# Kernel optimization log

Measured on AMD Instinct MI355X. Metric: run time of the kernel, lower is better.

## Reference

```python
import jax, jax.numpy as jnp
import numpy as np

EPS = 1e-12  # torch.nn.functional.normalize default eps


def sage_conv(x, src, dst, W_l, W_r, b, n_nodes):
    # PyG SAGEConv (mean aggr): out = lin_l(mean_{j in N(i)} x_j) + lin_r(x_i)
    # messages flow src -> dst
    agg = jax.ops.segment_sum(x[src], dst, num_segments=n_nodes)           # [N, d_in]
    cnt = jax.ops.segment_sum(jnp.ones_like(dst, dtype=x.dtype), dst,
                              num_segments=n_nodes)                         # [N]
    mean = agg / jnp.maximum(cnt, 1.0)[:, None]
    return mean @ W_l + x @ W_r + b


def l2_normalize(x):
    n = jnp.linalg.norm(x, axis=-1, keepdims=True)
    return x / jnp.maximum(n, EPS)


def setup_inputs() -> dict:
    key = jax.random.key(0)
    ks = jax.random.split(key, 16)
    N, E, G = 50000, 800000, 64
    d_in, d_h, d_out = 128, 128, 128

    x = jax.random.normal(ks[0], (N, d_in), dtype=jnp.float32)
    edge_index = jax.random.randint(ks[1], (2, E), 0, N, dtype=jnp.int32)
    batch = jnp.sort(jax.random.randint(ks[2], (N,), 0, G, dtype=jnp.int32))

    def lin(k, fan_in, fan_out):
        bound = 1.0 / np.sqrt(fan_in)
        return jax.random.uniform(k, (fan_in, fan_out), jnp.float32, -bound, bound)

    params = {
        "W_l1": lin(ks[3], d_in, d_h), "W_r1": lin(ks[4], d_in, d_h),
        "b1": jnp.zeros((d_h,), jnp.float32),
        "W_l2": lin(ks[5], d_h, d_h), "W_r2": lin(ks[6], d_h, d_h),
        "b2": jnp.zeros((d_h,), jnp.float32),
        "W_l3": lin(ks[7], d_h, d_out), "W_r3": lin(ks[8], d_h, d_out),
        "b3": jnp.zeros((d_out,), jnp.float32),
    }
    return {"x": x, "edge_index": edge_index, "batch": batch, **params}


def reference(x, edge_index, batch,
              W_l1, W_r1, b1, W_l2, W_r2, b2, W_l3, W_r3, b3):
    N = x.shape[0]
    G = 64  # number of graphs in the batch
    src, dst = edge_index[0], edge_index[1]

    h = jax.nn.relu(sage_conv(x, src, dst, W_l1, W_r1, b1, N))
    h = l2_normalize(h)
    h = jax.nn.relu(sage_conv(h, src, dst, W_l2, W_r2, b2, N))
    h = l2_normalize(h)
    h = sage_conv(h, src, dst, W_l3, W_r3, b3, N)
    h = l2_normalize(h)

    # global mean pool over graphs
    summed = jax.ops.segment_sum(h, batch, num_segments=G)                 # [G, d_out]
    counts = jax.ops.segment_sum(jnp.ones((N,), h.dtype), batch, num_segments=G)
    return summed / jnp.maximum(counts, 1.0)[:, None]
```

## Files before the change

### kernel.cpp

```cpp
#include <hip/hip_runtime.h>

#define N_NODES 50000
#define N_EDGES 800000
#define DIM 128
#define N_GRAPHS 64
#define NTILES 3125
#define NB 196
#define GPART 256
#define EPB 3125
#define XBF_BLKS 6250

typedef __attribute__((ext_vector_type(8))) short short8;
typedef __attribute__((ext_vector_type(4))) float f32x4;

__device__ __forceinline__ float bf2f(unsigned short h) {
  unsigned int u = ((unsigned int)h) << 16;
  return __builtin_bit_cast(float, u);
}
__device__ __forceinline__ unsigned short f2bf(float f) {
  unsigned int u = __builtin_bit_cast(unsigned int, f);
  u += 0x7FFFu + ((u >> 16) & 1u);
  return (unsigned short)(u >> 16);
}

__global__ __launch_bounds__(256) void k_front(
    const int* __restrict__ ei, int* __restrict__ cnt,
    const float* __restrict__ x, unsigned short* __restrict__ xbf,
    const float* __restrict__ w0, const float* __restrict__ w1,
    const float* __restrict__ w2, const float* __restrict__ w3,
    const float* __restrict__ w4, const float* __restrict__ w5,
    unsigned short* __restrict__ wfrag, float* __restrict__ out,
    const int* __restrict__ batch, float* __restrict__ inv_gcnt) {
  int blk = blockIdx.x, tid = threadIdx.x;
  if (blk < GPART) {
    __shared__ int h[NB];
    if (tid < NB) h[tid] = 0;
    __syncthreads();
    int e0 = blk * EPB;
    for (int i = tid; i < EPB; i += 256) {
      int dst = ei[N_EDGES + e0 + i];
      atomicAdd(&h[dst >> 8], 1);
    }
    __syncthreads();
    if (tid < NB) cnt[blk * NB + tid] = h[tid];
  } else if (blk < GPART + XBF_BLKS) {
    int i = (blk - GPART) * 256 + tid;
    if (i * 4 >= N_NODES * DIM) return;
    float4 v = ((const float4*)x)[i];
    unsigned int lo = (unsigned int)f2bf(v.x) | ((unsigned int)f2bf(v.y) << 16);
    unsigned int hi = (unsigned int)f2bf(v.z) | ((unsigned int)f2bf(v.w) << 16);
    uint2 o; o.x = lo; o.y = hi;
    ((uint2*)xbf)[i] = o;
  } else {
    int b = blk - GPART - XBF_BLKS;
    if (b < 48) {
      int idx = b * 256 + tid;
      int mat = idx >> 11;
      int rem = idx & 2047;
      int lane = rem & 63;
      int kk = (rem >> 6) & 3;
      int t = rem >> 8;
      const float* w = (mat == 0) ? w0 : (mat == 1) ? w1 : (mat == 2) ? w2
                     : (mat == 3) ? w3 : (mat == 4) ? w4 : w5;
      int row = t * 16 + (lane & 15);
      int k0 = kk * 32 + (lane >> 4) * 8;
      unsigned int v[8];
      #pragma unroll
      for (int j = 0; j < 8; ++j) v[j] = f2bf(w[(k0 + j) * DIM + row]);
      uint4 o;
      o.x = v[0] | (v[1] << 16);
      o.y = v[2] | (v[3] << 16);
      o.z = v[4] | (v[5] << 16);
      o.w = v[6] | (v[7] << 16);
      ((uint4*)wfrag)[idx] = o;
    } else if (b < 80) {
      int i = (b - 48) * 256 + tid;
      if (i < N_GRAPHS * DIM) out[i] = 0.f;
    } else {
      int g = tid;
      if (g >= N_GRAPHS) return;
      int lo = 0, hi = N_NODES;
      while (lo < hi) { int m = (lo + hi) >> 1; if (batch[m] < g) lo = m + 1; else hi = m; }
      int s = lo;
      lo = 0; hi = N_NODES;
      int g1 = g + 1;
      while (lo < hi) { int m = (lo + hi) >> 1; if (batch[m] < g1) lo = m + 1; else hi = m; }
      int c = lo - s;
      inv_gcnt[g] = 1.0f / (float)(c > 1 ? c : 1);
    }
  }
}


__global__ void k_escan(int* __restrict__ cnt, int* __restrict__ bb) {
  __shared__ int s[256];
  int t = threadIdx.x;
  int tot = 0;
  if (t < NB)
    for (int g = 0; g < GPART; ++g) tot += cnt[g * NB + t];
  s[t] = (t < NB) ? tot : 0;
  __syncthreads();
  for (int off = 1; off < 256; off <<= 1) {
    int v = (t >= off) ? s[t - off] : 0;
    __syncthreads();
    s[t] += v;
    __syncthreads();
  }
  if (t < NB) {
    int excl = s[t] - tot;
    bb[t] = excl;
    if (t == NB - 1) bb[NB] = s[t];
    int run = excl;
    for (int g = 0; g < GPART; ++g) {
      int c = cnt[g * NB + t];
      cnt[g * NB + t] = run;
      run += c;
    }
  }
}

__global__ __launch_bounds__(256) void k_bucket(const int* __restrict__ ei,
                                                const int* __restrict__ cnt,
                                                unsigned int* __restrict__ bucketed) {
  __shared__ int lofs[NB];
  int t = threadIdx.x, g = blockIdx.x;
  if (t < NB) lofs[t] = cnt[g * NB + t];
  __syncthreads();
  int e0 = g * EPB;
  for (int i = t; i < EPB; i += 256) {
    int src = ei[e0 + i];
    int dst = ei[N_EDGES + e0 + i];
    int p = atomicAdd(&lofs[dst >> 8], 1);
    bucketed[p] = (unsigned int)src | ((unsigned int)(dst & 255) << 16);
  }
}

__global__ __launch_bounds__(256) void k_finalize(const unsigned int* __restrict__ bucketed,
                                                  const int* __restrict__ bb,
                                                  int* __restrict__ rowptr,
                                                  int* __restrict__ col) {
  __shared__ int h[256], s[256], c[256];
  int t = threadIdx.x, b = blockIdx.x;
  int s0 = bb[b], s1 = bb[b + 1];
  int n = s1 - s0;
  h[t] = 0;
  __syncthreads();
  for (int i = t; i < n; i += 256) atomicAdd(&h[bucketed[s0 + i] >> 16], 1);
  __syncthreads();
  s[t] = h[t];
  __syncthreads();
  for (int off = 1; off < 256; off <<= 1) {
    int v = (t >= off) ? s[t - off] : 0;
    __syncthreads();
    s[t] += v;
    __syncthreads();
  }
  int excl = s[t] - h[t];
  int node = b * 256 + t;
  if (node < N_NODES) rowptr[node] = s0 + excl;
  if (b == NB - 1 && t == 255) rowptr[N_NODES] = N_EDGES;
  c[t] = s0 + excl;
  __syncthreads();
  for (int i = t; i < n; i += 256) {
    unsigned int v = bucketed[s0 + i];
    int p = atomicAdd(&c[v >> 16], 1);
    col[p] = (int)(v & 0xffffu);
  }
}


#define ACC8(V)                                   \
  a0 += bf2f((unsigned short)((V).x & 0xffff));   \
  a1 += bf2f((unsigned short)((V).x >> 16));      \
  a2 += bf2f((unsigned short)((V).y & 0xffff));   \
  a3 += bf2f((unsigned short)((V).y >> 16));      \
  a4 += bf2f((unsigned short)((V).z & 0xffff));   \
  a5 += bf2f((unsigned short)((V).z >> 16));      \
  a6 += bf2f((unsigned short)((V).w & 0xffff));   \
  a7 += bf2f((unsigned short)((V).w >> 16));

__global__ __launch_bounds__(256) void k_agg(const unsigned short* __restrict__ xin,
                                             const int* __restrict__ rowptr,
                                             const int* __restrict__ col,
                                             unsigned short* __restrict__ meanbf) {
  int wid = (blockIdx.x * blockDim.x + threadIdx.x) >> 6;
  int lane = threadIdx.x & 63;
  if (wid >= N_NODES) return;
  int start = rowptr[wid], end = rowptr[wid + 1];
  int g = lane >> 4;
  int li = lane & 15;

  float a0 = 0.f, a1 = 0.f, a2 = 0.f, a3 = 0.f;
  float a4 = 0.f, a5 = 0.f, a6 = 0.f, a7 = 0.f;
  for (int j0 = start; j0 < end; j0 += 64) {
    int m = end - j0;
    if (m > 64) m = 64;
    int idx = (lane < m) ? col[j0 + lane] : 0;
    int jj = g;
    if (jj < m) {
      int nb = __shfl(idx, jj);
      uint4 v = *(const uint4*)(xin + (size_t)nb * DIM + li * 8);
      jj += 4;
      if (jj < m) {
        int nb2 = __shfl(idx, jj);
        uint4 w = *(const uint4*)(xin + (size_t)nb2 * DIM + li * 8);
        for (jj += 4; jj < m; jj += 4) {
          int nb3 = __shfl(idx, jj);
          uint4 u = *(const uint4*)(xin + (size_t)nb3 * DIM + li * 8);
          ACC8(v);
          v = w;
          w = u;
        }
        ACC8(v);
        v = w;
      }
      ACC8(v);
    }
  }
  a0 += __shfl_xor(a0, 16); a0 += __shfl_xor(a0, 32);
  a1 += __shfl_xor(a1, 16); a1 += __shfl_xor(a1, 32);
  a2 += __shfl_xor(a2, 16); a2 += __shfl_xor(a2, 32);
  a3 += __shfl_xor(a3, 16); a3 += __shfl_xor(a3, 32);
  a4 += __shfl_xor(a4, 16); a4 += __shfl_xor(a4, 32);
  a5 += __shfl_xor(a5, 16); a5 += __shfl_xor(a5, 32);
  a6 += __shfl_xor(a6, 16); a6 += __shfl_xor(a6, 32);
  a7 += __shfl_xor(a7, 16); a7 += __shfl_xor(a7, 32);

  if (g == 0) {
    int d = end - start;
    float sc = 1.0f / (float)(d > 1 ? d : 1);
    uint4 o;
    o.x = (unsigned int)f2bf(a0 * sc) | ((unsigned int)f2bf(a1 * sc) << 16);
    o.y = (unsigned int)f2bf(a2 * sc) | ((unsigned int)f2bf(a3 * sc) << 16);
    o.z = (unsigned int)f2bf(a4 * sc) | ((unsigned int)f2bf(a5 * sc) << 16);
    o.w = (unsigned int)f2bf(a6 * sc) | ((unsigned int)f2bf(a7 * sc) << 16);
    *(uint4*)(meanbf + (size_t)wid * DIM + li * 8) = o;
  }
}

__global__ __launch_bounds__(512) void k_gemm(const unsigned short* __restrict__ meanbf,
                                              const unsigned short* __restrict__ xin,
                                              const unsigned short* __restrict__ wfragL,
                                              const unsigned short* __restrict__ wfragR,
                                              const float* __restrict__ bias,
                                              unsigned short* __restrict__ outbf,
                                              int relu,
                                              const int* __restrict__ batch,
                                              const float* __restrict__ inv_gcnt,
                                              float* __restrict__ pool_out) {
  __shared__ __align__(16) unsigned short wl[8 * 4 * 64 * 8];
  __shared__ __align__(16) unsigned short wr[8 * 4 * 64 * 8];
  const int tid = threadIdx.x;
  int wave = tid >> 6;
  int lane = tid & 63;
  int tb = blockIdx.x * 8 + wave;
  int lg = lane >> 4;
  int li = lane & 15;

  short8 am[4], ax[4];
  {
    int tbc = (tb < NTILES) ? tb : (NTILES - 1);
    const unsigned short* mrow = meanbf + ((size_t)(tbc * 16 + li)) * DIM + lg * 8;
    const unsigned short* xrow = xin + ((size_t)(tbc * 16 + li)) * DIM + lg * 8;
    #pragma unroll
    for (int kk = 0; kk < 4; ++kk) {
      am[kk] = *(const short8*)(mrow + kk * 32);
      ax[kk] = *(const short8*)(xrow + kk * 32);
    }
  }

  {
    const uint4* gl = (const uint4*)wfragL;
    const uint4* gr = (const uint4*)wfragR;
    uint4* sl = (uint4*)wl;
    uint4* sr = (uint4*)wr;
    #pragma unroll
    for (int i = 0; i < 4; ++i) {
      sl[tid + 512 * i] = gl[tid + 512 * i];
      sr[tid + 512 * i] = gr[tid + 512 * i];
    }
  }
  __syncthreads();
  if (tb >= NTILES) return;

  f32x4 acc[8];
  #pragma unroll
  for (int t = 0; t < 8; ++t) {
    f32x4 c = {0.f, 0.f, 0.f, 0.f};
    #pragma unroll
    for (int kk = 0; kk < 4; ++kk) {
      short8 bl = *(const short8*)(wl + (((t * 4 + kk) * 64 + lane) * 8));
      c = __builtin_amdgcn_mfma_f32_16x16x32_bf16(am[kk], bl, c, 0, 0, 0);
      short8 br = *(const short8*)(wr + (((t * 4 + kk) * 64 + lane) * 8));
      c = __builtin_amdgcn_mfma_f32_16x16x32_bf16(ax[kk], br, c, 0, 0, 0);
    }
    float bv = bias[t * 16 + li];
    #pragma unroll
    for (int r = 0; r < 4; ++r) {
      float v = c[r] + bv;
      if (relu) v = fmaxf(v, 0.f);
      c[r] = v;
    }
    acc[t] = c;
  }

  float scale[4];
  #pragma unroll
  for (int r = 0; r < 4; ++r) {
    float s = 0.f;
    #pragma unroll
    for (int t = 0; t < 8; ++t) s += acc[t][r] * acc[t][r];
    s += __shfl_xor(s, 1);
    s += __shfl_xor(s, 2);
    s += __shfl_xor(s, 4);
    s += __shfl_xor(s, 8);
    float n = sqrtf(s);
    scale[r] = 1.0f / fmaxf(n, 1e-12f);
  }

  if (pool_out) {
    int rowbase = tb * 16 + lg * 4;
    int bg[4];
    #pragma unroll
    for (int r = 0; r < 4; ++r) bg[r] = batch[rowbase + r];
    int g_cur = batch[tb * 16];
    while (true) {
      float p[8];
      #pragma unroll
      for (int t = 0; t < 8; ++t) {
        float s = 0.f;
        #pragma unroll
        for (int r = 0; r < 4; ++r)
          if (bg[r] == g_cur) s += acc[t][r] * scale[r];
        p[t] = s;
      }
      #pragma unroll
      for (int t = 0; t < 8; ++t) {
        p[t] += __shfl_xor(p[t], 16);
        p[t] += __shfl_xor(p[t], 32);
      }
      if (lg == 0) {
        float inv = inv_gcnt[g_cur];
        #pragma unroll
        for (int t = 0; t < 8; ++t)
          atomicAdd(&pool_out[g_cur * DIM + t * 16 + li], p[t] * inv);
      }
      int nxt = 0x7fffffff;
      #pragma unroll
      for (int r = 0; r < 4; ++r)
        if (bg[r] > g_cur && bg[r] < nxt) nxt = bg[r];
      nxt = min(nxt, __shfl_xor(nxt, 16));
      nxt = min(nxt, __shfl_xor(nxt, 32));
      if (nxt == 0x7fffffff) break;
      g_cur = nxt;
    }
  } else {
    #pragma unroll
    for (int t = 0; t < 8; ++t) {
      #pragma unroll
      for (int r = 0; r < 4; ++r) {
        outbf[((size_t)(tb * 16 + lg * 4 + r)) * DIM + t * 16 + li] =
            f2bf(acc[t][r] * scale[r]);
      }
    }
  }
}


extern "C" void kernel_launch(void* const* d_in, const int* in_sizes, int n_in,
                              void* d_out, int out_size, void* d_ws, size_t ws_size,
                              hipStream_t stream) {
  const float* x   = (const float*)d_in[0];
  const int* ei    = (const int*)d_in[1];
  const int* batch = (const int*)d_in[2];
  const float* Wl1 = (const float*)d_in[3];
  const float* Wr1 = (const float*)d_in[4];
  const float* b1  = (const float*)d_in[5];
  const float* Wl2 = (const float*)d_in[6];
  const float* Wr2 = (const float*)d_in[7];
  const float* b2  = (const float*)d_in[8];
  const float* Wl3 = (const float*)d_in[9];
  const float* Wr3 = (const float*)d_in[10];
  const float* b3  = (const float*)d_in[11];
  float* out = (float*)d_out;

  char* ws = (char*)d_ws;
  size_t off = 0;
  auto alloc = [&](size_t bytes) {
    void* p = ws + off;
    off += (bytes + 255) & ~(size_t)255;
    return p;
  };
  unsigned short* xbf   = (unsigned short*)alloc((size_t)N_NODES * DIM * 2);
  unsigned short* hB    = (unsigned short*)alloc((size_t)N_NODES * DIM * 2);
  unsigned short* hC    = (unsigned short*)alloc((size_t)N_NODES * DIM * 2);
  unsigned short* mean  = (unsigned short*)alloc((size_t)N_NODES * DIM * 2);
  unsigned short* wfrag = (unsigned short*)alloc((size_t)6 * 2048 * 16);
  int* rowptr = (int*)alloc((size_t)(N_NODES + 1) * 4);
  int* col    = (int*)alloc((size_t)N_EDGES * 4);
  int* cnt    = (int*)alloc((size_t)GPART * NB * 4);
  int* bb     = (int*)alloc((size_t)(NB + 1) * 4);
  unsigned int* bucketed = (unsigned int*)alloc((size_t)N_EDGES * 4);
  float* inv_gcnt = (float*)alloc((size_t)N_GRAPHS * 4);

  k_front<<<GPART + XBF_BLKS + 81, 256, 0, stream>>>(
      ei, cnt, x, xbf, Wl1, Wr1, Wl2, Wr2, Wl3, Wr3, wfrag, out, batch, inv_gcnt);

  k_escan<<<1, 256, 0, stream>>>(cnt, bb);
  k_bucket<<<GPART, 256, 0, stream>>>(ei, cnt, bucketed);
  k_finalize<<<NB, 256, 0, stream>>>(bucketed, bb, rowptr, col);

  k_agg<<<12500, 256, 0, stream>>>(xbf, rowptr, col, mean);
  k_gemm<<<391, 512, 0, stream>>>(mean, xbf, wfrag + 0 * 16384, wfrag + 1 * 16384,
                                  b1, hB, 1, batch, inv_gcnt, nullptr);
  k_agg<<<12500, 256, 0, stream>>>(hB, rowptr, col, mean);
  k_gemm<<<391, 512, 0, stream>>>(mean, hB, wfrag + 2 * 16384, wfrag + 3 * 16384,
                                  b2, hC, 1, batch, inv_gcnt, nullptr);
  k_agg<<<12500, 256, 0, stream>>>(hC, rowptr, col, mean);
  k_gemm<<<391, 512, 0, stream>>>(mean, hC, wfrag + 4 * 16384, wfrag + 5 * 16384,
                                  b3, nullptr, 0, batch, inv_gcnt, out);
}
```

Before: 169.5 us.

## Fuse neighbor aggregation and MFMA GEMM into one per-layer kernel

Merges the aggregation and GEMM kernels into a single per-layer kernel. Each 1024-thread block has 16 waves that each aggregate one node into padded shared memory; wave 0 then runs the MFMA GEMM for that 16-row tile, reading weight fragments straight from global memory instead of staging them in LDS. This removes the round trip of the mean buffer through global memory and one launch per layer, and deepens the gather prefetch pipeline by one stage. In exchange, 15 of 16 waves sit idle during the GEMM phase and weight fragments are re-read from global or cache by every block.

```diff
diff --git a/kernel.cpp b/kernel.cpp
--- a/kernel.cpp
+++ b/kernel.cpp
@@ -9,6 +9,7 @@
 #define GPART 256
 #define EPB 3125
 #define XBF_BLKS 6250
+#define PADB 272
 
 typedef __attribute__((ext_vector_type(8))) short short8;
 typedef __attribute__((ext_vector_type(4))) float f32x4;
@@ -179,109 +180,89 @@
   a6 += bf2f((unsigned short)((V).w & 0xffff));   \
   a7 += bf2f((unsigned short)((V).w >> 16));
 
-__global__ __launch_bounds__(256) void k_agg(const unsigned short* __restrict__ xin,
-                                             const int* __restrict__ rowptr,
-                                             const int* __restrict__ col,
-                                             unsigned short* __restrict__ meanbf) {
-  int wid = (blockIdx.x * blockDim.x + threadIdx.x) >> 6;
-  int lane = threadIdx.x & 63;
-  if (wid >= N_NODES) return;
-  int start = rowptr[wid], end = rowptr[wid + 1];
-  int g = lane >> 4;
-  int li = lane & 15;
-
-  float a0 = 0.f, a1 = 0.f, a2 = 0.f, a3 = 0.f;
-  float a4 = 0.f, a5 = 0.f, a6 = 0.f, a7 = 0.f;
-  for (int j0 = start; j0 < end; j0 += 64) {
-    int m = end - j0;
-    if (m > 64) m = 64;
-    int idx = (lane < m) ? col[j0 + lane] : 0;
-    int jj = g;
-    if (jj < m) {
-      int nb = __shfl(idx, jj);
-      uint4 v = *(const uint4*)(xin + (size_t)nb * DIM + li * 8);
-      jj += 4;
+__global__ __launch_bounds__(1024, 8) void k_layer(
+    const unsigned short* __restrict__ xin, const int* __restrict__ rowptr,
+    const int* __restrict__ col, const unsigned short* __restrict__ wfragL,
+    const unsigned short* __restrict__ wfragR, const float* __restrict__ bias,
+    unsigned short* __restrict__ outbf, int relu,
+    const int* __restrict__ batch, const float* __restrict__ inv_gcnt,
+    float* __restrict__ pool_out) {
+  __shared__ __align__(16) unsigned char smean[16 * PADB];
+  const int tid = threadIdx.x;
+  const int wave = tid >> 6, lane = tid & 63;
+  const int tb = blockIdx.x;
+
+  {
+    int node = tb * 16 + wave;
+    int start = rowptr[node], end = rowptr[node + 1];
+    int g = lane >> 4;
+    int li = lane & 15;
+    float a0 = 0.f, a1 = 0.f, a2 = 0.f, a3 = 0.f;
+    float a4 = 0.f, a5 = 0.f, a6 = 0.f, a7 = 0.f;
+    for (int j0 = start; j0 < end; j0 += 64) {
+      int m = end - j0;
+      if (m > 64) m = 64;
+      int idx = (lane < m) ? col[j0 + lane] : 0;
+      int jj = g;
       if (jj < m) {
-        int nb2 = __shfl(idx, jj);
-        uint4 w = *(const uint4*)(xin + (size_t)nb2 * DIM + li * 8);
-        for (jj += 4; jj < m; jj += 4) {
-          int nb3 = __shfl(idx, jj);
-          uint4 u = *(const uint4*)(xin + (size_t)nb3 * DIM + li * 8);
+        int nb = __shfl(idx, jj);
+        uint4 v = *(const uint4*)(xin + (size_t)nb * DIM + li * 8);
+        jj += 4;
+        if (jj < m) {
+          int nb2 = __shfl(idx, jj);
+          uint4 w = *(const uint4*)(xin + (size_t)nb2 * DIM + li * 8);
+          jj += 4;
+          if (jj < m) {
+            int nb3 = __shfl(idx, jj);
+            uint4 u = *(const uint4*)(xin + (size_t)nb3 * DIM + li * 8);
+            for (jj += 4; jj < m; jj += 4) {
+              int nb4 = __shfl(idx, jj);
+              uint4 z = *(const uint4*)(xin + (size_t)nb4 * DIM + li * 8);
+              ACC8(v);
+              v = w; w = u; u = z;
+            }
+            ACC8(v);
+            v = w; w = u;
+          }
           ACC8(v);
           v = w;
-          w = u;
         }
         ACC8(v);
-        v = w;
       }
-      ACC8(v);
-    }
-  }
-  a0 += __shfl_xor(a0, 16); a0 += __shfl_xor(a0, 32);
-  a1 += __shfl_xor(a1, 16); a1 += __shfl_xor(a1, 32);
-  a2 += __shfl_xor(a2, 16); a2 += __shfl_xor(a2, 32);
-  a3 += __shfl_xor(a3, 16); a3 += __shfl_xor(a3, 32);
-  a4 += __shfl_xor(a4, 16); a4 += __shfl_xor(a4, 32);
-  a5 += __shfl_xor(a5, 16); a5 += __shfl_xor(a5, 32);
-  a6 += __shfl_xor(a6, 16); a6 += __shfl_xor(a6, 32);
-  a7 += __shfl_xor(a7, 16); a7 += __shfl_xor(a7, 32);
-
-  if (g == 0) {
-    int d = end - start;
-    float sc = 1.0f / (float)(d > 1 ? d : 1);
-    uint4 o;
-    o.x = (unsigned int)f2bf(a0 * sc) | ((unsigned int)f2bf(a1 * sc) << 16);
-    o.y = (unsigned int)f2bf(a2 * sc) | ((unsigned int)f2bf(a3 * sc) << 16);
-    o.z = (unsigned int)f2bf(a4 * sc) | ((unsigned int)f2bf(a5 * sc) << 16);
-    o.w = (unsigned int)f2bf(a6 * sc) | ((unsigned int)f2bf(a7 * sc) << 16);
-    *(uint4*)(meanbf + (size_t)wid * DIM + li * 8) = o;
-  }
-}
-
-__global__ __launch_bounds__(512) void k_gemm(const unsigned short* __restrict__ meanbf,
-                                              const unsigned short* __restrict__ xin,
-                                              const unsigned short* __restrict__ wfragL,
-                                              const unsigned short* __restrict__ wfragR,
-                                              const float* __restrict__ bias,
-                                              unsigned short* __restrict__ outbf,
-                                              int relu,
-                                              const int* __restrict__ batch,
-                                              const float* __restrict__ inv_gcnt,
-                                              float* __restrict__ pool_out) {
-  __shared__ __align__(16) unsigned short wl[8 * 4 * 64 * 8];
-  __shared__ __align__(16) unsigned short wr[8 * 4 * 64 * 8];
-  const int tid = threadIdx.x;
-  int wave = tid >> 6;
-  int lane = tid & 63;
-  int tb = blockIdx.x * 8 + wave;
-  int lg = lane >> 4;
-  int li = lane & 15;
+    }
+    a0 += __shfl_xor(a0, 16); a0 += __shfl_xor(a0, 32);
+    a1 += __shfl_xor(a1, 16); a1 += __shfl_xor(a1, 32);
+    a2 += __shfl_xor(a2, 16); a2 += __shfl_xor(a2, 32);
+    a3 += __shfl_xor(a3, 16); a3 += __shfl_xor(a3, 32);
+    a4 += __shfl_xor(a4, 16); a4 += __shfl_xor(a4, 32);
+    a5 += __shfl_xor(a5, 16); a5 += __shfl_xor(a5, 32);
+    a6 += __shfl_xor(a6, 16); a6 += __shfl_xor(a6, 32);
+    a7 += __shfl_xor(a7, 16); a7 += __shfl_xor(a7, 32);
+    if (g == 0) {
+      int d = end - start;
+      float sc = 1.0f / (float)(d > 1 ? d : 1);
+      uint4 o;
+      o.x = (unsigned int)f2bf(a0 * sc) | ((unsigned int)f2bf(a1 * sc) << 16);
+      o.y = (unsigned int)f2bf(a2 * sc) | ((unsigned int)f2bf(a3 * sc) << 16);
+      o.z = (unsigned int)f2bf(a4 * sc) | ((unsigned int)f2bf(a5 * sc) << 16);
+      o.w = (unsigned int)f2bf(a6 * sc) | ((unsigned int)f2bf(a7 * sc) << 16);
+      *(uint4*)(smean + wave * PADB + li * 16) = o;
+    }
+  }
+  __syncthreads();
+  if (wave != 0) return;
+
+  const int lg = lane >> 4;
+  const int li = lane & 15;
 
   short8 am[4], ax[4];
-  {
-    int tbc = (tb < NTILES) ? tb : (NTILES - 1);
-    const unsigned short* mrow = meanbf + ((size_t)(tbc * 16 + li)) * DIM + lg * 8;
-    const unsigned short* xrow = xin + ((size_t)(tbc * 16 + li)) * DIM + lg * 8;
-    #pragma unroll
-    for (int kk = 0; kk < 4; ++kk) {
-      am[kk] = *(const short8*)(mrow + kk * 32);
-      ax[kk] = *(const short8*)(xrow + kk * 32);
-    }
-  }
-
-  {
-    const uint4* gl = (const uint4*)wfragL;
-    const uint4* gr = (const uint4*)wfragR;
-    uint4* sl = (uint4*)wl;
-    uint4* sr = (uint4*)wr;
-    #pragma unroll
-    for (int i = 0; i < 4; ++i) {
-      sl[tid + 512 * i] = gl[tid + 512 * i];
-      sr[tid + 512 * i] = gr[tid + 512 * i];
-    }
-  }
-  __syncthreads();
-  if (tb >= NTILES) return;
+  const unsigned char* arow = smean + (size_t)li * PADB + lg * 16;
+  const unsigned short* xrow = xin + ((size_t)(tb * 16 + li)) * DIM + lg * 8;
+  #pragma unroll
+  for (int kk = 0; kk < 4; ++kk) {
+    am[kk] = *(const short8*)(arow + kk * 64);
+    ax[kk] = *(const short8*)(xrow + kk * 32);
+  }
 
   f32x4 acc[8];
   #pragma unroll
@@ -289,9 +270,9 @@
     f32x4 c = {0.f, 0.f, 0.f, 0.f};
     #pragma unroll
     for (int kk = 0; kk < 4; ++kk) {
-      short8 bl = *(const short8*)(wl + (((t * 4 + kk) * 64 + lane) * 8));
+      short8 bl = *(const short8*)(wfragL + (((t * 4 + kk) * 64 + lane) * 8));
       c = __builtin_amdgcn_mfma_f32_16x16x32_bf16(am[kk], bl, c, 0, 0, 0);
-      short8 br = *(const short8*)(wr + (((t * 4 + kk) * 64 + lane) * 8));
+      short8 br = *(const short8*)(wfragR + (((t * 4 + kk) * 64 + lane) * 8));
       c = __builtin_amdgcn_mfma_f32_16x16x32_bf16(ax[kk], br, c, 0, 0, 0);
     }
     float bv = bias[t * 16 + li];
@@ -394,7 +375,6 @@
   unsigned short* xbf   = (unsigned short*)alloc((size_t)N_NODES * DIM * 2);
   unsigned short* hB    = (unsigned short*)alloc((size_t)N_NODES * DIM * 2);
   unsigned short* hC    = (unsigned short*)alloc((size_t)N_NODES * DIM * 2);
-  unsigned short* mean  = (unsigned short*)alloc((size_t)N_NODES * DIM * 2);
   unsigned short* wfrag = (unsigned short*)alloc((size_t)6 * 2048 * 16);
   int* rowptr = (int*)alloc((size_t)(N_NODES + 1) * 4);
   int* col    = (int*)alloc((size_t)N_EDGES * 4);
@@ -410,13 +390,13 @@
   k_bucket<<<GPART, 256, 0, stream>>>(ei, cnt, bucketed);
   k_finalize<<<NB, 256, 0, stream>>>(bucketed, bb, rowptr, col);
 
-  k_agg<<<12500, 256, 0, stream>>>(xbf, rowptr, col, mean);
-  k_gemm<<<391, 512, 0, stream>>>(mean, xbf, wfrag + 0 * 16384, wfrag + 1 * 16384,
-                                  b1, hB, 1, batch, inv_gcnt, nullptr);
-  k_agg<<<12500, 256, 0, stream>>>(hB, rowptr, col, mean);
-  k_gemm<<<391, 512, 0, stream>>>(mean, hB, wfrag + 2 * 16384, wfrag + 3 * 16384,
-                                  b2, hC, 1, batch, inv_gcnt, nullptr);
-  k_agg<<<12500, 256, 0, stream>>>(hC, rowptr, col, mean);
-  k_gemm<<<391, 512, 0, stream>>>(mean, hC, wfrag + 4 * 16384, wfrag + 5 * 16384,
-                                  b3, nullptr, 0, batch, inv_gcnt, out);
-}
+  k_layer<<<NTILES, 1024, 0, stream>>>(xbf, rowptr, col, wfrag + 0 * 16384,
+                                       wfrag + 1 * 16384, b1, hB, 1,
+                                       batch, inv_gcnt, nullptr);
+  k_layer<<<NTILES, 1024, 0, stream>>>(hB, rowptr, col, wfrag + 2 * 16384,
+                                       wfrag + 3 * 16384, b2, hC, 1,
+                                       batch, inv_gcnt, nullptr);
+  k_layer<<<NTILES, 1024, 0, stream>>>(hC, rowptr, col, wfrag + 4 * 16384,
+                                       wfrag + 5 * 16384, b3, nullptr, 0,
+                                       batch, inv_gcnt, out);
+}
```

New measurement: 211.8 us. +24.9%, slower.
